# Kernel tuning notes

Hardware: AMD Instinct MI355X
Metric: run time of the kernel (lower is better)

## Reference

```python
import jax, jax.numpy as jnp
import numpy as np

N, D, NUM_CLASSES = 8192, 256, 512
DELTA = 1.0


def setup_inputs() -> dict:
    key = jax.random.key(0)
    k1, k2 = jax.random.split(key)
    queries = jax.random.normal(k1, (N, D), dtype=jnp.float32)
    targets = jax.random.randint(k2, (N,), 0, NUM_CLASSES, dtype=jnp.int64)
    return {"queries": queries, "targets": targets}


def _mine(queries, targets):
    # Pairwise squared L2 distances via gram expansion (avoids [N,N,D] intermediate).
    sq = jnp.sum(queries * queries, axis=-1)              # [N]
    dist = sq[:, None] + sq[None, :] - 2.0 * (queries @ queries.T)  # [N,N]
    same = targets[:, None] == targets[None, :]           # [N,N] bool
    diag = jnp.eye(dist.shape[0], dtype=bool)
    neg_inf = jnp.float32(-jnp.inf)
    # hardest positive: argmax over (distances * same_mask) with -inf diagonal
    pos_masked = jnp.where(diag, neg_inf, dist * same)
    pos_idx = jnp.argmax(pos_masked, axis=-1)
    # original: (-(distances * ~same, diag=-inf)).argmin == argmax of the masked matrix
    neg_masked = jnp.where(diag, neg_inf, dist * (~same))
    neg_idx = jnp.argmax(neg_masked, axis=-1)
    return pos_idx, neg_idx


def reference(queries, targets):
    pos_idx, neg_idx = _mine(queries, targets)
    pos = queries[pos_idx]                                # [N,D]
    neg = queries[neg_idx]                                # [N,D]
    d_pos = jnp.sum((queries - pos) ** 2, axis=-1, keepdims=True)  # [N,1]
    d_neg = jnp.sum((queries - neg) ** 2, axis=-1, keepdims=True)  # [N,1]
    loss = jax.nn.relu(DELTA - d_pos + d_neg)
    return jnp.mean(loss)
```

## Files before the change

kernel.cpp:

```cpp
#include <hip/hip_runtime.h>

#define N 8192
#define D 256
#define NB 64
#define NTILES (NB * (NB + 1) / 2)

typedef float f32x4 __attribute__((ext_vector_type(4)));
typedef long long i64;

__device__ __forceinline__ void gload16(const void* g, void* lds) {
    __builtin_amdgcn_global_load_lds(
        (const __attribute__((address_space(1))) void*)g,
        (__attribute__((address_space(3))) void*)lds, 16, 0, 0);
}


__global__ __launch_bounds__(256) void prep_kernel(const float* __restrict__ q,
                                                   unsigned char* __restrict__ q8,
                                                   float* __restrict__ sq,
                                                   unsigned* __restrict__ pos_key,
                                                   unsigned* __restrict__ neg_key,
                                                   float* __restrict__ out) {
    const int row = blockIdx.x * 4 + (threadIdx.x >> 6);
    const int lane = threadIdx.x & 63;
    if (threadIdx.x < 8) {
        const int r0 = blockIdx.x * 4 + (threadIdx.x >> 1);
        if (threadIdx.x & 1) neg_key[r0] = 0u; else pos_key[r0] = 0u;
    }
    if (blockIdx.x == 0 && threadIdx.x == 0) out[0] = 0.0f;
    const float4 v = ((const float4*)(q + row * D))[lane];
    int r = 0;
    r = __builtin_amdgcn_cvt_pk_fp8_f32(v.x, v.y, r, false);
    r = __builtin_amdgcn_cvt_pk_fp8_f32(v.z, v.w, r, true);
    ((int*)(q8 + (size_t)row * D))[lane] = r;
    float s = v.x * v.x + v.y * v.y + v.z * v.z + v.w * v.w;
    #pragma unroll
    for (int off = 32; off; off >>= 1) s += __shfl_down(s, off, 64);
    if (lane == 0) sq[row] = s;
}

__global__ __launch_bounds__(256, 3) void mine_kernel(
    const unsigned char* __restrict__ q8, const int* __restrict__ tgt,
    const float* __restrict__ sqv,
    unsigned* __restrict__ pos_key, unsigned* __restrict__ neg_key)
{
    __shared__ __align__(16) char smem[65536];
    __shared__ float sqI[128], sqJ[128];
    __shared__ int   tgI[128], tgJ[128];

    int tt = blockIdx.x, bi = 0;
    while (tt >= NB - bi) { tt -= NB - bi; ++bi; }
    const int bj = bi + tt;
    const int i0 = bi * 128, j0 = bj * 128;
    const bool diag = (bi == bj);

    const int tid = threadIdx.x;
    const int w = tid >> 6, lane = tid & 63;
    const int quad = lane >> 4, lc = lane & 15;
    const int wy = w >> 1, wx = w & 1;

    if (tid < 128) { sqI[tid] = sqv[i0 + tid]; tgI[tid] = tgt[i0 + tid]; }
    else { const int c = tid - 128; sqJ[c] = sqv[j0 + c]; tgJ[c] = tgt[j0 + c]; }

    #pragma unroll
    for (int c = 0; c < 4; ++c) {
        #pragma unroll
        for (int it = 0; it < 2; ++it) {
            const int s = it * 256 + tid;
            const int r = s >> 2, bo = (s & 3) * 16;
            const int lbase = c * 8192 + (it * 256 + w * 64) * 16;
            gload16(q8 + (size_t)(i0 + r) * D + c * 64 + bo, smem + lbase);
            if (!diag)
                gload16(q8 + (size_t)(j0 + r) * D + c * 64 + bo,
                        smem + 32768 + lbase);
        }
    }
    __syncthreads();

    float sqjn[4];
    #pragma unroll
    for (int nt = 0; nt < 4; ++nt) sqjn[nt] = sqJ[wx * 64 + nt * 16 + lc];
    f32x4 acc[4][4];
    #pragma unroll
    for (int mt = 0; mt < 4; ++mt) {
        const f32x4 si4 = *(const f32x4*)&sqI[wy * 64 + mt * 16 + quad * 4];
        #pragma unroll
        for (int nt = 0; nt < 4; ++nt)
            #pragma unroll
            for (int r = 0; r < 4; ++r)
                acc[mt][nt][r] = -0.5f * (si4[r] + sqjn[nt]);
    }

    for (int c = 0; c < 4; ++c) {
        const char* AP = smem + c * 8192;
        const char* BP = diag ? AP : smem + 32768 + c * 8192;
        union { int4 v; i64 d[2]; } fb[4], fa;
        #pragma unroll
        for (int t = 0; t < 4; ++t)
            fb[t].v = *(const int4*)(BP + (wx * 64 + t * 16 + lc) * 64 + quad * 16);
        #pragma unroll
        for (int mt = 0; mt < 4; ++mt) {
            fa.v = *(const int4*)(AP + (wy * 64 + mt * 16 + lc) * 64 + quad * 16);
            #pragma unroll
            for (int nt = 0; nt < 4; ++nt) {
                acc[mt][nt] = __builtin_amdgcn_mfma_f32_16x16x32_fp8_fp8(
                    fa.d[0], fb[nt].d[0], acc[mt][nt], 0, 0, 0);
                acc[mt][nt] = __builtin_amdgcn_mfma_f32_16x16x32_fp8_fp8(
                    fa.d[1], fb[nt].d[1], acc[mt][nt], 0, 0, 0);
            }
        }
    }
    __syncthreads();

    unsigned* const mpos = (unsigned*)smem;
    unsigned* const mneg = mpos + 128 * 33;

    int tj[4]; unsigned jc[4], jpk[4], jnk[4];
    #pragma unroll
    for (int nt = 0; nt < 4; ++nt) {
        const int cl = wx * 64 + nt * 16 + lc;
        tj[nt] = tgJ[cl];
        jc[nt] = 0x1FFFu - (unsigned)(j0 + cl);
        jpk[nt] = 0u; jnk[nt] = 0u;
    }

    #pragma unroll
    for (int mt = 0; mt < 4; ++mt) {
        const int rbase = wy * 64 + mt * 16 + quad * 4;
        const int4 ti4 = *(const int4*)&tgI[rbase];
        #pragma unroll
        for (int r = 0; r < 4; ++r) {
            const int sr = rbase + r;
            const unsigned rk = 0x1FFFu - (unsigned)(i0 + sr);
            const int ti = ((const int*)&ti4)[r];
            unsigned bpk = 0u, bnk = 0u;
            if (!diag) {
                #pragma unroll
                for (int nt = 0; nt < 4; ++nt) {
                    const float dist = fmaxf(-2.0f * acc[mt][nt][r], 0.0f);
                    const unsigned db = __float_as_uint(dist) & 0xFFFFE000u;
                    const bool same = (ti == tj[nt]);
                    const unsigned ki = db | jc[nt];
                    const unsigned pi_ = same ? ki : 0u;
                    bpk = max(bpk, pi_);
                    bnk = max(bnk, ki - pi_);
                    const unsigned kj = db | rk;
                    const unsigned pj_ = same ? kj : 0u;
                    jpk[nt] = max(jpk[nt], pj_);
                    jnk[nt] = max(jnk[nt], kj - pj_);
                }
            } else {
                #pragma unroll
                for (int nt = 0; nt < 4; ++nt) {
                    const int cl = wx * 64 + nt * 16 + lc;
                    const float dist = fmaxf(-2.0f * acc[mt][nt][r], 0.0f);
                    const unsigned db = (sr == cl) ? 0u
                        : (__float_as_uint(dist) & 0xFFFFE000u);
                    const bool same = (ti == tj[nt]);
                    const unsigned ki = db | jc[nt];
                    const unsigned pi_ = same ? ki : 0u;
                    bpk = max(bpk, pi_);
                    bnk = max(bnk, ki - pi_);
                }
            }
            mpos[sr * 33 + wx * 16 + lc] = bpk;
            mneg[sr * 33 + wx * 16 + lc] = bnk;
        }
    }
    __syncthreads();

    {
        const int sr = tid & 127;
        const unsigned* m = (tid < 128) ? &mpos[sr * 33] : &mneg[sr * 33];
        unsigned best = 0u;
        #pragma unroll
        for (int k = 0; k < 32; ++k) best = max(best, m[k]);
        unsigned* gk = (tid < 128) ? pos_key : neg_key;
        atomicMax(&gk[i0 + sr], best);
    }

    if (!diag) {
        #pragma unroll
        for (int nt = 0; nt < 4; ++nt) {
            unsigned pk = jpk[nt], nk = jnk[nt];
            #pragma unroll
            for (int off = 16; off < 64; off <<= 1) {
                pk = max(pk, (unsigned)__shfl_xor((int)pk, off, 64));
                nk = max(nk, (unsigned)__shfl_xor((int)nk, off, 64));
            }
            if (quad == 0) {
                const int gcol = j0 + wx * 64 + nt * 16 + lc;
                atomicMax(&pos_key[gcol], pk);
                atomicMax(&neg_key[gcol], nk);
            }
        }
    }
}

__global__ __launch_bounds__(256) void final_kernel(
    const float* __restrict__ q, const unsigned* __restrict__ pos_key,
    const unsigned* __restrict__ neg_key, float* __restrict__ out)
{
    __shared__ float red[4];
    const int wv = threadIdx.x >> 6, lane = threadIdx.x & 63;
    float wsum = 0.0f;
    for (int rr = 0; rr < 32; ++rr) {
        const int row = (blockIdx.x * 4 + wv) * 32 + rr;
        const int bpi = 0x1FFF - (int)(pos_key[row] & 0x1FFFu);
        const int bni = 0x1FFF - (int)(neg_key[row] & 0x1FFFu);
        const float4 qi = ((const float4*)(q + row * D))[lane];
        const float4 qp = ((const float4*)(q + (size_t)bpi * D))[lane];
        const float4 qn = ((const float4*)(q + (size_t)bni * D))[lane];
        float dx, dp = 0.0f, dn = 0.0f;
        dx = qi.x - qp.x; dp += dx * dx;
        dx = qi.y - qp.y; dp += dx * dx;
        dx = qi.z - qp.z; dp += dx * dx;
        dx = qi.w - qp.w; dp += dx * dx;
        dx = qi.x - qn.x; dn += dx * dx;
        dx = qi.y - qn.y; dn += dx * dx;
        dx = qi.z - qn.z; dn += dx * dx;
        dx = qi.w - qn.w; dn += dx * dx;
        #pragma unroll
        for (int off = 32; off; off >>= 1) {
            dp += __shfl_down(dp, off, 64);
            dn += __shfl_down(dn, off, 64);
        }
        if (lane == 0) wsum += fmaxf(0.0f, (1.0f - dp) + dn);
    }
    if (lane == 0) red[wv] = wsum;
    __syncthreads();
    if (threadIdx.x == 0)
        atomicAdd(out, (red[0] + red[1] + red[2] + red[3]) * (1.0f / N));
}

extern "C" void kernel_launch(void* const* d_in, const int* in_sizes, int n_in,
                              void* d_out, int out_size, void* d_ws, size_t ws_size,
                              hipStream_t stream) {
    const float* q = (const float*)d_in[0];
    const int* tgt = (const int*)d_in[1];
    float* out = (float*)d_out;

    unsigned* pos_key = (unsigned*)d_ws;
    unsigned* neg_key = pos_key + N;
    unsigned char* q8 = (unsigned char*)(neg_key + N);
    float* sqv = (float*)(q8 + (size_t)N * D);

    prep_kernel<<<dim3(N / 4), dim3(256), 0, stream>>>(q, q8, sqv, pos_key, neg_key, out);
    mine_kernel<<<dim3(NTILES), dim3(256), 0, stream>>>(q8, tgt, sqv, pos_key, neg_key);
    final_kernel<<<dim3(64), dim3(256), 0, stream>>>(q, pos_key, neg_key, out);
}
```

Before: 112.2 us.

## Stage the fp8 K dimension in two halves to halve LDS footprint

Instead of loading all 256 fp8 columns of both row tiles into a 64 KB shared buffer, the kernel loads the first 128 columns, runs the MFMAs, then reloads the second half into the same space. The shared buffer is resized to fit the later argmax scratch arrays (about 33 KB). The goal is to let more blocks be resident per CU so global loads and compute of different blocks overlap. The cost is an extra pair of barriers and a serialized reload inside each block, with no double-buffering.

```diff
diff --git a/kernel.cpp b/kernel.cpp
--- a/kernel.cpp
+++ b/kernel.cpp
@@ -44,9 +44,10 @@
     const float* __restrict__ sqv,
     unsigned* __restrict__ pos_key, unsigned* __restrict__ neg_key)
 {
-    __shared__ __align__(16) char smem[65536];
+    __shared__ __align__(16) unsigned Msh[2 * 128 * 33];
     __shared__ float sqI[128], sqJ[128];
     __shared__ int   tgI[128], tgJ[128];
+    char* const smem = (char*)Msh;
 
     int tt = blockIdx.x, bi = 0;
     while (tt >= NB - bi) { tt -= NB - bi; ++bi; }
@@ -62,17 +63,20 @@
     if (tid < 128) { sqI[tid] = sqv[i0 + tid]; tgI[tid] = tgt[i0 + tid]; }
     else { const int c = tid - 128; sqJ[c] = sqv[j0 + c]; tgJ[c] = tgt[j0 + c]; }
 
-    #pragma unroll
-    for (int c = 0; c < 4; ++c) {
+    const int sr_ = tid >> 2;
+    const int bo_ = (tid & 3) * 16;
+    const int lb_ = (w * 64) * 16;
+
+    #pragma unroll
+    for (int c2 = 0; c2 < 2; ++c2) {
         #pragma unroll
         for (int it = 0; it < 2; ++it) {
-            const int s = it * 256 + tid;
-            const int r = s >> 2, bo = (s & 3) * 16;
-            const int lbase = c * 8192 + (it * 256 + w * 64) * 16;
-            gload16(q8 + (size_t)(i0 + r) * D + c * 64 + bo, smem + lbase);
+            const int r = sr_ + it * 64;
+            const int lbase = c2 * 8192 + it * 4096 + lb_;
+            gload16(q8 + (size_t)(i0 + r) * D + c2 * 64 + bo_, smem + lbase);
             if (!diag)
-                gload16(q8 + (size_t)(j0 + r) * D + c * 64 + bo,
-                        smem + 32768 + lbase);
+                gload16(q8 + (size_t)(j0 + r) * D + c2 * 64 + bo_,
+                        smem + 16384 + lbase);
         }
     }
     __syncthreads();
@@ -91,29 +95,50 @@
                 acc[mt][nt][r] = -0.5f * (si4[r] + sqjn[nt]);
     }
 
-    for (int c = 0; c < 4; ++c) {
-        const char* AP = smem + c * 8192;
-        const char* BP = diag ? AP : smem + 32768 + c * 8192;
-        union { int4 v; i64 d[2]; } fb[4], fa;
-        #pragma unroll
-        for (int t = 0; t < 4; ++t)
-            fb[t].v = *(const int4*)(BP + (wx * 64 + t * 16 + lc) * 64 + quad * 16);
-        #pragma unroll
-        for (int mt = 0; mt < 4; ++mt) {
-            fa.v = *(const int4*)(AP + (wy * 64 + mt * 16 + lc) * 64 + quad * 16);
-            #pragma unroll
-            for (int nt = 0; nt < 4; ++nt) {
-                acc[mt][nt] = __builtin_amdgcn_mfma_f32_16x16x32_fp8_fp8(
-                    fa.d[0], fb[nt].d[0], acc[mt][nt], 0, 0, 0);
-                acc[mt][nt] = __builtin_amdgcn_mfma_f32_16x16x32_fp8_fp8(
-                    fa.d[1], fb[nt].d[1], acc[mt][nt], 0, 0, 0);
-            }
-        }
-    }
-    __syncthreads();
-
-    unsigned* const mpos = (unsigned*)smem;
-    unsigned* const mneg = mpos + 128 * 33;
+    #pragma unroll
+    for (int p = 0; p < 2; ++p) {
+        #pragma unroll
+        for (int c2 = 0; c2 < 2; ++c2) {
+            const char* AP = smem + c2 * 8192;
+            const char* BP = diag ? AP : smem + 16384 + c2 * 8192;
+            union { int4 v; i64 d[2]; } fb[4], fa;
+            #pragma unroll
+            for (int t = 0; t < 4; ++t)
+                fb[t].v = *(const int4*)(BP + (wx * 64 + t * 16 + lc) * 64 + quad * 16);
+            #pragma unroll
+            for (int mt = 0; mt < 4; ++mt) {
+                fa.v = *(const int4*)(AP + (wy * 64 + mt * 16 + lc) * 64 + quad * 16);
+                #pragma unroll
+                for (int nt = 0; nt < 4; ++nt) {
+                    acc[mt][nt] = __builtin_amdgcn_mfma_f32_16x16x32_fp8_fp8(
+                        fa.d[0], fb[nt].d[0], acc[mt][nt], 0, 0, 0);
+                    acc[mt][nt] = __builtin_amdgcn_mfma_f32_16x16x32_fp8_fp8(
+                        fa.d[1], fb[nt].d[1], acc[mt][nt], 0, 0, 0);
+                }
+            }
+        }
+        if (p == 0) {
+            __syncthreads();
+            #pragma unroll
+            for (int c2 = 0; c2 < 2; ++c2) {
+                #pragma unroll
+                for (int it = 0; it < 2; ++it) {
+                    const int r = sr_ + it * 64;
+                    const int lbase = c2 * 8192 + it * 4096 + lb_;
+                    gload16(q8 + (size_t)(i0 + r) * D + 128 + c2 * 64 + bo_,
+                            smem + lbase);
+                    if (!diag)
+                        gload16(q8 + (size_t)(j0 + r) * D + 128 + c2 * 64 + bo_,
+                                smem + 16384 + lbase);
+                }
+            }
+            __syncthreads();
+        }
+    }
+    __syncthreads();
+
+    unsigned* const mpos = Msh;
+    unsigned* const mneg = Msh + 128 * 33;
 
     int tj[4]; unsigned jc[4], jpk[4], jnk[4];
     #pragma unroll
```

New measurement: 107.3 us. 1.05x faster.
